# Kernel optimization log

Measured on AMD Instinct MI355X. Metric: run time of the kernel, lower is better.

Reference implementation:

```python
import jax, jax.numpy as jnp
import numpy as np

EPS = 1e-5
BLOCK = 16

def setup_inputs() -> dict:
    key = jax.random.key(0)
    ks = jax.random.split(key, 5)
    B, S, D = 8, 4096, 1024
    G = D // BLOCK            # 64 groups
    sq = int(np.sqrt(D))      # 32
    x = jax.random.normal(ks[0], (B, S, D), dtype=jnp.float32)
    gamma = jnp.ones((D,), jnp.float32)
    beta = jnp.zeros((D,), jnp.float32)
    block_weights = 0.5 * jax.random.normal(ks[1], (G, BLOCK, BLOCK), dtype=jnp.float32)
    W_row = 0.1 * jax.random.normal(ks[2], (sq, sq), dtype=jnp.float32)
    W_col = 0.1 * jax.random.normal(ks[3], (sq, sq), dtype=jnp.float32)
    alpha = jnp.float32(0.3)
    bias = jnp.zeros((D,), jnp.float32)
    return {"x": x, "gamma": gamma, "beta": beta, "block_weights": block_weights,
            "W_row": W_row, "W_col": W_col, "alpha": alpha, "bias": bias}

def reference(x, gamma, beta, block_weights, W_row, W_col, alpha, bias):
    D = x.shape[-1]
    G, Bk, _ = block_weights.shape      # 64, 16, 16 (D == G*Bk, no pad)
    sq = W_row.shape[0]                 # 32 (D == sq*sq, no pad)
    # LayerNorm (fp32)
    mu = jnp.mean(x, axis=-1, keepdims=True)
    var = jnp.mean(jnp.square(x - mu), axis=-1, keepdims=True)
    xn = (x - mu) * jax.lax.rsqrt(var + EPS) * gamma + beta
    x_flat = xn.reshape(-1, D)          # [N, D]
    # Block-diagonal mix: [N, G, Bk] x [G, Bk, Bk]
    xg = x_flat.reshape(-1, G, Bk)
    y = jnp.einsum('ngb,gbc->ngc', xg, block_weights).reshape(-1, D)
    block_out = jnp.flip(y, axis=-1)
    # Monarch path: [N, sq, sq] @ W_col @ W_row^T
    xgrid = x_flat.reshape(-1, sq, sq)
    z = jnp.einsum('nrc,ck,sk->nrs', xgrid, W_col, W_row).reshape(-1, D)
    out = block_out + alpha * z + bias
    return out.reshape(x.shape)
```

## Files before the change

kernel.cpp:

```cpp
#include <hip/hip_runtime.h>

typedef __bf16 bf16x8 __attribute__((ext_vector_type(8)));
typedef __bf16 bf16x4 __attribute__((ext_vector_type(4)));
typedef float f32x4 __attribute__((ext_vector_type(4)));

#define EPS 1e-5f

__global__ __launch_bounds__(256) void hbsl_precompute(
    const float* __restrict__ bw, const float* __restrict__ W_row,
    const float* __restrict__ W_col, const float* __restrict__ alpha_p,
    __bf16* __restrict__ mt, __bf16* __restrict__ bwt)
{
    const int t = threadIdx.x;
    if (blockIdx.x == 0) {
        const float alpha = alpha_p[0];
        #pragma unroll
        for (int k = 0; k < 4; ++k) {
            int flat = t + 256 * k;
            int s = flat >> 5, c = flat & 31;
            float acc = 0.f;
            #pragma unroll 8
            for (int kk = 0; kk < 32; ++kk)
                acc += W_col[c * 32 + kk] * W_row[s * 32 + kk];
            mt[s * 32 + c] = (__bf16)(alpha * acc);
        }
    } else {
        int g = blockIdx.x - 1;
        int c = t >> 4, b = t & 15;
        bwt[g * 256 + c * 16 + b] = (__bf16)bw[g * 256 + b * 16 + c];
    }
}

__global__ __launch_bounds__(256) void hbsl_main(
    const float* __restrict__ x, const float* __restrict__ gamma,
    const float* __restrict__ beta, const float* __restrict__ bias,
    const __bf16* __restrict__ mt, const __bf16* __restrict__ bwt,
    float* __restrict__ out)
{
    __shared__ __bf16 xn[16 * 1032];
    const int t = threadIdx.x;
    const int lane = t & 63;
    const int wv = t >> 6;
    const int q = lane >> 4, n = lane & 15;
    const int row = t >> 4, li = t & 15;
    const int rbase = blockIdx.x * 16;

    bf16x8 mfrag0 = *(const bf16x8*)(mt + n * 32 + q * 8);
    bf16x8 mfrag1 = *(const bf16x8*)(mt + (16 + n) * 32 + q * 8);

    const float* xr = x + (rbase + row) * 1024;
    float4 xv[16];
    float s = 0.f, ss = 0.f;
    #pragma unroll
    for (int i = 0; i < 16; ++i) {
        xv[i] = *(const float4*)(xr + li * 4 + i * 64);
        s += xv[i].x + xv[i].y + xv[i].z + xv[i].w;
        ss += xv[i].x * xv[i].x + xv[i].y * xv[i].y
            + xv[i].z * xv[i].z + xv[i].w * xv[i].w;
    }
    #pragma unroll
    for (int m = 1; m < 16; m <<= 1) {
        s  += __shfl_xor(s, m, 64);
        ss += __shfl_xor(ss, m, 64);
    }
    const float mu = s * (1.f / 1024.f);
    const float rstd = rsqrtf(ss * (1.f / 1024.f) - mu * mu + EPS);
    #pragma unroll
    for (int i = 0; i < 16; ++i) {
        const int col = li * 4 + i * 64;
        float4 g4 = *(const float4*)(gamma + col);
        float4 b4 = *(const float4*)(beta + col);
        bf16x4 v;
        v[0] = (__bf16)((xv[i].x - mu) * rstd * g4.x + b4.x);
        v[1] = (__bf16)((xv[i].y - mu) * rstd * g4.y + b4.y);
        v[2] = (__bf16)((xv[i].z - mu) * rstd * g4.z + b4.z);
        v[3] = (__bf16)((xv[i].w - mu) * rstd * g4.w + b4.w);
        *(bf16x4*)(&xn[row * 1032 + col]) = v;
    }
    __syncthreads();

    bf16x8 bz;
    #pragma unroll
    for (int i = 0; i < 8; ++i) bz[i] = (__bf16)0.f;
    const f32x4 zf = {0.f, 0.f, 0.f, 0.f};

    #pragma unroll
    for (int p = 0; p < 8; ++p) {
        const int o0 = wv * 16 + 2 * p;
        const int r  = o0 >> 1;
        const int gp = 31 - r;
        const int g_odd  = 2 * gp + 1;
        const int g_even = 2 * gp;

        bf16x8 az = *(const bf16x8*)(&xn[n * 1032 + r  * 32 + q * 8]);
        bf16x8 ay = *(const bf16x8*)(&xn[n * 1032 + gp * 32 + q * 8]);

        bf16x8 by0 = bz, by1 = bz;
        if (q >= 2) by0 = *(const bf16x8*)(bwt + g_odd  * 256 + (15 - n) * 16 + (q - 2) * 8);
        else        by1 = *(const bf16x8*)(bwt + g_even * 256 + (15 - n) * 16 + q * 8);

        f32x4 z0 = __builtin_amdgcn_mfma_f32_16x16x32_bf16(az, mfrag0, zf, 0, 0, 0);
        f32x4 z1 = __builtin_amdgcn_mfma_f32_16x16x32_bf16(az, mfrag1, zf, 0, 0, 0);
        f32x4 y0 = __builtin_amdgcn_mfma_f32_16x16x32_bf16(ay, by0, zf, 0, 0, 0);
        f32x4 y1 = __builtin_amdgcn_mfma_f32_16x16x32_bf16(ay, by1, zf, 0, 0, 0);

        const float bias0 = bias[o0 * 16 + n];
        const float bias1 = bias[o0 * 16 + 16 + n];
        float* op = out + (rbase + q * 4) * 1024 + o0 * 16 + n;
        #pragma unroll
        for (int rg = 0; rg < 4; ++rg) {
            op[rg * 1024]      = y0[rg] + z0[rg] + bias0;
            op[rg * 1024 + 16] = y1[rg] + z1[rg] + bias1;
        }
    }
}

extern "C" void kernel_launch(void* const* d_in, const int* in_sizes, int n_in,
                              void* d_out, int out_size, void* d_ws, size_t ws_size,
                              hipStream_t stream) {
    const float* x      = (const float*)d_in[0];
    const float* gamma  = (const float*)d_in[1];
    const float* beta   = (const float*)d_in[2];
    const float* bw     = (const float*)d_in[3];
    const float* W_row  = (const float*)d_in[4];
    const float* W_col  = (const float*)d_in[5];
    const float* alpha  = (const float*)d_in[6];
    const float* bias   = (const float*)d_in[7];
    float* o = (float*)d_out;

    __bf16* mt  = (__bf16*)d_ws;
    __bf16* bwt = (__bf16*)((char*)d_ws + 2048);

    const int N = in_sizes[0] / 1024;

    hipLaunchKernelGGL(hbsl_precompute, dim3(65), dim3(256), 0, stream,
                       bw, W_row, W_col, alpha, mt, bwt);
    hipLaunchKernelGGL(hbsl_main, dim3(N / 16), dim3(256), 0, stream,
                       x, gamma, beta, bias, mt, bwt, o);
}
```

Baseline: 262.8 us.

## Transpose MFMA operands for vectorized float4 output stores, prefetch weights and bias

Swaps the A/B operands of the MFMAs so each lane holds four consecutive output columns of one row, which lets the output go out as 16-byte float4 stores instead of scalar strided stores. Block-weight fragments are preloaded into registers before the LayerNorm phase, and bias is staged in shared memory. A min-blocks hint of 4 is added to launch bounds. The cost is more registers and extra LDS use, which could limit occupancy.

```diff
diff --git a/kernel.cpp b/kernel.cpp
--- a/kernel.cpp
+++ b/kernel.cpp
@@ -31,13 +31,14 @@
     }
 }
 
-__global__ __launch_bounds__(256) void hbsl_main(
+__global__ __launch_bounds__(256, 4) void hbsl_main(
     const float* __restrict__ x, const float* __restrict__ gamma,
     const float* __restrict__ beta, const float* __restrict__ bias,
     const __bf16* __restrict__ mt, const __bf16* __restrict__ bwt,
     float* __restrict__ out)
 {
     __shared__ __bf16 xn[16 * 1032];
+    __shared__ float bias_s[1024];
     const int t = threadIdx.x;
     const int lane = t & 63;
     const int wv = t >> 6;
@@ -48,7 +49,19 @@
     bf16x8 mfrag0 = *(const bf16x8*)(mt + n * 32 + q * 8);
     bf16x8 mfrag1 = *(const bf16x8*)(mt + (16 + n) * 32 + q * 8);
 
-    const float* xr = x + (rbase + row) * 1024;
+    bf16x8 bwf[8];
+    #pragma unroll
+    for (int p = 0; p < 8; ++p) {
+        const int o0 = wv * 16 + 2 * p;
+        const int gp = 31 - (o0 >> 1);
+        const int g = (q >= 2) ? (2 * gp + 1) : (2 * gp);
+        const int e = (q >= 2) ? (q - 2) * 8 : q * 8;
+        bwf[p] = *(const bf16x8*)(bwt + g * 256 + (15 - n) * 16 + e);
+    }
+
+    *(float4*)(&bias_s[t * 4]) = *(const float4*)(bias + t * 4);
+
+    const float* xr = x + (size_t)(rbase + row) * 1024;
     float4 xv[16];
     float s = 0.f, ss = 0.f;
     #pragma unroll
@@ -89,29 +102,24 @@
         const int o0 = wv * 16 + 2 * p;
         const int r  = o0 >> 1;
         const int gp = 31 - r;
-        const int g_odd  = 2 * gp + 1;
-        const int g_even = 2 * gp;
 
         bf16x8 az = *(const bf16x8*)(&xn[n * 1032 + r  * 32 + q * 8]);
         bf16x8 ay = *(const bf16x8*)(&xn[n * 1032 + gp * 32 + q * 8]);
 
-        bf16x8 by0 = bz, by1 = bz;
-        if (q >= 2) by0 = *(const bf16x8*)(bwt + g_odd  * 256 + (15 - n) * 16 + (q - 2) * 8);
-        else        by1 = *(const bf16x8*)(bwt + g_even * 256 + (15 - n) * 16 + q * 8);
+        bf16x8 a0 = (q >= 2) ? bwf[p] : bz;
+        bf16x8 a1 = (q <  2) ? bwf[p] : bz;
 
-        f32x4 z0 = __builtin_amdgcn_mfma_f32_16x16x32_bf16(az, mfrag0, zf, 0, 0, 0);
-        f32x4 z1 = __builtin_amdgcn_mfma_f32_16x16x32_bf16(az, mfrag1, zf, 0, 0, 0);
-        f32x4 y0 = __builtin_amdgcn_mfma_f32_16x16x32_bf16(ay, by0, zf, 0, 0, 0);
-        f32x4 y1 = __builtin_amdgcn_mfma_f32_16x16x32_bf16(ay, by1, zf, 0, 0, 0);
+        f32x4 z0 = __builtin_amdgcn_mfma_f32_16x16x32_bf16(mfrag0, az, zf, 0, 0, 0);
+        f32x4 z1 = __builtin_amdgcn_mfma_f32_16x16x32_bf16(mfrag1, az, zf, 0, 0, 0);
+        f32x4 y0 = __builtin_amdgcn_mfma_f32_16x16x32_bf16(a0, ay, zf, 0, 0, 0);
+        f32x4 y1 = __builtin_amdgcn_mfma_f32_16x16x32_bf16(a1, ay, zf, 0, 0, 0);
 
-        const float bias0 = bias[o0 * 16 + n];
-        const float bias1 = bias[o0 * 16 + 16 + n];
-        float* op = out + (rbase + q * 4) * 1024 + o0 * 16 + n;
-        #pragma unroll
-        for (int rg = 0; rg < 4; ++rg) {
-            op[rg * 1024]      = y0[rg] + z0[rg] + bias0;
-            op[rg * 1024 + 16] = y1[rg] + z1[rg] + bias1;
-        }
+        f32x4 b0 = *(const f32x4*)(&bias_s[o0 * 16 + q * 4]);
+        f32x4 b1 = *(const f32x4*)(&bias_s[o0 * 16 + 16 + q * 4]);
+
+        float* op = out + (size_t)(rbase + n) * 1024 + o0 * 16 + q * 4;
+        *(f32x4*)op        = y0 + z0 + b0;
+        *(f32x4*)(op + 16) = y1 + z1 + b1;
     }
 }
 
```

New measurement: 258.2 us. Within noise of the previous version (-1.8%).
